# Kernel optimization log

Hardware: AMD Instinct MI355X
Metric: run time of the kernel (lower is better)

Reference implementation:

```python
import jax, jax.numpy as jnp
import numpy as np

N = 100000       # nodes
D_IN = 256       # input feature dim
HID = 128        # hidden dim (GCN output)
D_OUT = 64       # SGCL output dim
NNZ = 1600000    # nnz of gcn adjacency
E = 500000       # directed edges (adj_e)
BIE = 1000000    # bidirectional edges (adj_n)


def setup_inputs() -> dict:
    key = jax.random.key(0)
    ks = jax.random.split(key, 13)
    X = jax.random.normal(ks[0], (N, D_IN), jnp.float32)
    # weight scales chosen so exp(logstd) stays well-conditioned (glorot-like)
    W_gcn = jax.random.normal(ks[1], (D_IN, HID), jnp.float32) * 0.05
    W_miu = jax.random.normal(ks[2], (2 * HID, D_OUT), jnp.float32) * 0.01
    W_sigma = jax.random.normal(ks[3], (2 * HID, D_OUT), jnp.float32) * 0.01
    gcn_values = jax.random.uniform(ks[4], (NNZ,), jnp.float32)
    bi_values = jax.random.uniform(ks[5], (BIE,), jnp.float32)
    noise_in = jax.random.normal(ks[6], (E, D_OUT), jnp.float32)
    noise_out = jax.random.normal(ks[7], (E, D_OUT), jnp.float32)
    noise_node = jax.random.normal(ks[8], (N, D_OUT), jnp.float32)
    gcn_indices = jax.random.randint(ks[9], (2, NNZ), 0, N)
    di_edges = jax.random.randint(ks[10], (2, E), 0, N)
    # ensure every node has at least one incident bi-edge (source side) so that
    # log(aggregated variance) is finite, as with a real symmetric adjacency
    bi_src = jnp.concatenate([jnp.arange(N), jax.random.randint(ks[11], (BIE - N,), 0, N)])
    bi_dst = jax.random.randint(ks[12], (BIE,), 0, N)
    bi_edges = jnp.stack([bi_src, bi_dst], axis=0)
    return {
        "X": X, "W_gcn": W_gcn, "W_miu": W_miu, "W_sigma": W_sigma,
        "gcn_values": gcn_values, "bi_values": bi_values,
        "noise_in": noise_in, "noise_out": noise_out, "noise_node": noise_node,
        "gcn_indices": gcn_indices, "di_edges": di_edges, "bi_edges": bi_edges,
    }


def reference(X, W_gcn, W_miu, W_sigma, gcn_values, bi_values,
              noise_in, noise_out, noise_node, gcn_indices, di_edges, bi_edges):
    n = X.shape[0]
    hid = W_gcn.shape[1]
    # ---- GraphConvSparse with identity activation: adj @ (X @ W) ----
    xw = X @ W_gcn                                     # [N, HID]
    msgs = gcn_values[:, None] * xw[gcn_indices[1]]    # [NNZ, HID]
    hidden = jax.ops.segment_sum(msgs, gcn_indices[0], num_segments=n)
    # split weights: concat([h_a, h_b]) @ W == h_a @ W_top + h_b @ W_bot
    Wm_t, Wm_b = W_miu[:hid], W_miu[hid:]
    Ws_t, Ws_b = W_sigma[:hid], W_sigma[hid:]
    # ---- edge embedding (directed edges) ----
    h_src = hidden[di_edges[0]]                        # [E, HID]
    h_dst = hidden[di_edges[1]]                        # [E, HID]
    miu_in = h_src @ Wm_t + h_dst @ Wm_b               # [E, D_OUT]
    miu_out = h_dst @ Wm_t + h_src @ Wm_b
    logstd_in = h_src @ Ws_t + h_dst @ Ws_b
    logstd_out = h_dst @ Ws_t + h_src @ Ws_b
    edge_in = noise_in * jnp.exp(logstd_in) + miu_in
    edge_out = noise_out * jnp.exp(logstd_out) + miu_out
    # ---- node embedding (bidirectional edges, weighted scatter-aggregate) ----
    b0 = hidden[bi_edges[0]]                           # [BIE, HID]
    b1 = hidden[bi_edges[1]]
    bi_miu = b0 @ Wm_t + b1 @ Wm_b                     # [BIE, D_OUT]
    bi_logstd = b0 @ Ws_t + b1 @ Ws_b
    node_miu = jax.ops.segment_sum(bi_values[:, None] * bi_miu, bi_edges[0], num_segments=n)
    node_var = jax.ops.segment_sum((bi_values ** 2)[:, None] * jnp.exp(bi_logstd), bi_edges[0], num_segments=n)
    node_logstd = 0.5 * jnp.log(node_var)
    node_embed = noise_node * jnp.exp(node_logstd) + node_miu
    return (node_embed, edge_in, edge_out)
```

## Files before the change

kernel.cpp:

```cpp
#include <hip/hip_runtime.h>
#include <hip/hip_bf16.h>
#include <string.h>

typedef unsigned short u16t;
typedef unsigned int   u32t;
typedef unsigned long long u64t;

#define NNODE 100000
#define DIN   256
#define HIDN  128
#define DOUTN 64
#define NNZE  1600000
#define EDIR  500000
#define EBI   1000000
#define G64   1563
#define NBIN  782
#define CH3   4096
#define K3G   391
#define K3B   245
#define KPART (K3G+K3B)
#define CAPG  2432
#define CAPB  1536
#define EBLK  15625

typedef __attribute__((ext_vector_type(8))) short bf16x8;
typedef __attribute__((ext_vector_type(4))) float f32x4;
typedef __attribute__((ext_vector_type(4))) float f4v;

__device__ __forceinline__ u32t pk2bf(float a, float b){
  __hip_bfloat162 h = __float22bfloat162_rn(make_float2(a, b));
  union { __hip_bfloat162 h2; u32t u; } c; c.h2 = h; return c.u;
}
__device__ __forceinline__ u16t s2bf(float a){
  __hip_bfloat16 h = __float2bfloat16(a);
  union { __hip_bfloat16 h1; u16t u; } c; c.h1 = h; return c.u;
}
__device__ __forceinline__ float2 up2(u32t w){
  return make_float2(__uint_as_float(w<<16), __uint_as_float(w&0xFFFF0000u));
}

__global__ __launch_bounds__(256) void histprep_kernel(const int* __restrict__ gi,
                                                       const int* __restrict__ be,
                                                       u32t* __restrict__ gcnt_c,
                                                       u32t* __restrict__ bcnt_c,
                                                       const float* __restrict__ Wg,
                                                       const float* __restrict__ Wm,
                                                       const float* __restrict__ Wsg,
                                                       u16t* __restrict__ Wg_pre,
                                                       u16t* __restrict__ Wc_pre){
  __shared__ u32t h[1024];
  int blk = blockIdx.x, t = threadIdx.x;
  if(blk >= KPART){
    int idx = (blk-KPART)*256 + t;
    int e = idx & 7, l = (idx>>3) & 63, f = (idx>>9) & 63, sel = idx>>15;
    int k_in = ((e>>2)<<4) + ((l>>4)<<2) + (e&3);
    if(sel == 0){
      int ks = f>>3, nf = f&7;
      int k = ks*32 + k_in, n = nf*16 + (l&15);
      Wg_pre[idx] = s2bf(Wg[(size_t)k*HIDN + n]);
    } else {
      int ks = f>>4, nf = f&15;
      int k = ks*32 + k_in, c = nf*16 + (l&15);
      int half = c>>7, ci = c&127;
      const float* src = (ci&1) ? Wsg : Wm;
      Wc_pre[idx - 32768] = s2bf(src[(size_t)(half*128 + k)*DOUTN + (ci>>1)]);
    }
    return;
  }
  const int* keys; u32t* outc; int E, e0;
  if(blk < K3G){ keys=gi; outc=gcnt_c; E=NNZE; e0=blk*CH3; }
  else         { keys=be; outc=bcnt_c; E=EBI;  e0=(blk-K3G)*CH3; }
  for(int i=t;i<1024;i+=256) h[i]=0;
  __syncthreads();
  for(int i=t;i<CH3;i+=256){
    int e=e0+i;
    if(e<E) atomicAdd(&h[(u32t)keys[e]>>7], 1u);
  }
  __syncthreads();
  for(int b=t;b<1024;b+=256){
    u32t c=h[b];
    if(c) atomicAdd(&outc[b], c);
  }
}

__global__ __launch_bounds__(256) void scan_coarse_kernel(u32t* __restrict__ gcnt_c,
                                                          u32t* __restrict__ gcoff,
                                                          u32t* __restrict__ gcur_,
                                                          u32t* __restrict__ bcnt_c,
                                                          u32t* __restrict__ bcoff,
                                                          u32t* __restrict__ bcur_){
  __shared__ u32t part[256];
  u32t *cnt, *coff, *cur;
  if(blockIdx.x==0){ cnt=gcnt_c; coff=gcoff; cur=gcur_; }
  else             { cnt=bcnt_c; coff=bcoff; cur=bcur_; }
  int t = threadIdx.x;
  u32t ch[4], s=0;
  #pragma unroll
  for(int j=0;j<4;j++){ int idx=t*4+j; ch[j] = (idx<NBIN)? cnt[idx] : 0u; s+=ch[j]; }
  part[t]=s; __syncthreads();
  for(int off=1;off<256;off<<=1){
    u32t x=(t>=off)?part[t-off]:0u;
    __syncthreads();
    part[t]+=x;
    __syncthreads();
  }
  u32t run=(t==0)?0u:part[t-1];
  #pragma unroll
  for(int j=0;j<4;j++){
    int idx=t*4+j;
    if(idx<NBIN){ coff[idx]=run; cur[idx]=run; run+=ch[j]; }
  }
  if(t==255) coff[NBIN]=part[255];
}

__global__ __launch_bounds__(256) void partgemm1_kernel(const float* __restrict__ X,
                                                        const u16t* __restrict__ Wg_pre,
                                                        u16t* __restrict__ xwb,
                                                        const int* __restrict__ gi,
                                                        const float* __restrict__ gv,
                                                        const int* __restrict__ be,
                                                        const float* __restrict__ bv,
                                                        u32t* __restrict__ gcur_,
                                                        u64t* __restrict__ gbuck,
                                                        u32t* __restrict__ bcur_,
                                                        u64t* __restrict__ bbuck){
  __shared__ __align__(16) char smem[50176];
  const int t = threadIdx.x;
  if(blockIdx.x < G64){
    u16t* Xs = (u16t*)smem;
    const int l = t & 63, w = t >> 6;
    const int row0 = blockIdx.x * 64;
    for(int i=0;i<16;i++){
      int m = w*16 + i;
      int mg = min(row0 + m, NNODE-1);
      f4v f = __builtin_nontemporal_load((const f4v*)&X[(size_t)mg*DIN + l*4]);
      u32t* p = (u32t*)&Xs[m*256 + ((l ^ (m&15))<<2)];
      p[0] = pk2bf(f[0], f[1]);
      p[1] = pk2bf(f[2], f[3]);
    }
    __syncthreads();
    f32x4 acc[8];
    #pragma unroll
    for(int nf=0;nf<8;nf++) acc[nf] = (f32x4)(0.f);
    const int lm = l & 15, l4 = l >> 4;
    const int mrow = w*16 + lm;
    #pragma unroll 1
    for(int ks=0; ks<8; ks++){
      int kg = ks*8 + l4;
      union { uint2 u2[2]; bf16x8 v; } a;
      a.u2[0] = *(const uint2*)&Xs[mrow*256 + ((kg     ^ lm)<<2)];
      a.u2[1] = *(const uint2*)&Xs[mrow*256 + (((kg+4) ^ lm)<<2)];
      #pragma unroll
      for(int nf=0;nf<8;nf++){
        union { uint4 u4; bf16x8 v; } b;
        b.u4 = *(const uint4*)&Wg_pre[(size_t)((ks*8+nf)*64 + l)*8];
        acc[nf] = __builtin_amdgcn_mfma_f32_16x16x32_bf16(a.v, b.v, acc[nf], 0, 0, 0);
      }
    }
    #pragma unroll
    for(int r=0;r<4;r++){
      int gr = row0 + w*16 + l4*4 + r;
      if(gr < NNODE){
        #pragma unroll
        for(int nf=0;nf<8;nf++)
          xwb[(size_t)gr*HIDN + nf*16 + lm] = s2bf(acc[nf][r]);
      }
    }
    return;
  }
  u32t* hist = (u32t*)smem;
  u32t* scn  = (u32t*)(smem+4096);
  u32t* prt  = (u32t*)(smem+8192);
  u64t* ebuf = (u64t*)(smem+9216);
  u16t* bins = (u16t*)(smem+41984);
  int blk = blockIdx.x - G64;
  const int *keys, *pay; const float* val; u32t* cursor; u64t* buck; int E, e0;
  if(blk < K3G){ keys=gi; pay=gi+NNZE; val=gv; cursor=gcur_; buck=gbuck; E=NNZE; e0=blk*CH3; }
  else         { keys=be; pay=be+EBI;  val=bv; cursor=bcur_; buck=bbuck; E=EBI;  e0=(blk-K3G)*CH3; }
  for(int i=t;i<1024;i+=256) hist[i]=0;
  __syncthreads();
  for(int i=t;i<CH3;i+=256){
    int e=e0+i;
    if(e<E) atomicAdd(&hist[(u32t)keys[e]>>7], 1u);
  }
  __syncthreads();
  u32t ch[4], s=0;
  #pragma unroll
  for(int j=0;j<4;j++){ ch[j]=hist[t*4+j]; s+=ch[j]; }
  prt[t]=s; __syncthreads();
  for(int off=1;off<256;off<<=1){
    u32t x=(t>=off)?prt[t-off]:0u;
    __syncthreads();
    prt[t]+=x;
    __syncthreads();
  }
  u32t run=(t==0)?0u:prt[t-1];
  #pragma unroll
  for(int j=0;j<4;j++){ scn[t*4+j]=run; run+=ch[j]; }
  __syncthreads();
  for(int i=t;i<1024;i+=256) hist[i]=scn[i];
  __syncthreads();
  for(int i=t;i<CH3;i+=256){
    int e=e0+i;
    if(e<E){
      int k = keys[e];
      u32t b = (u32t)k>>7;
      u32t p = atomicAdd(&hist[b],1u);
      u64t ent = (u64t)((u32t)pay[e] | (((u32t)k&127u)<<20)) | ((u64t)__float_as_uint(val[e])<<32);
      ebuf[p]=ent; bins[p]=(u16t)b;
    }
  }
  __syncthreads();
  for(int b=t;b<1024;b+=256){
    u32t c = hist[b]-scn[b];
    u32t bs = c ? atomicAdd(&cursor[b], c) : 0u;
    hist[b] = bs;
  }
  __syncthreads();
  int totalValid = prt[255];
  for(int i=t;i<totalValid;i+=256){
    u32t b = bins[i];
    buck[ (size_t)hist[b] + (u32t)i - scn[b] ] = ebuf[i];
  }
}

__global__ __launch_bounds__(256) void gcn_gather2_kernel(const u16t* __restrict__ xwb,
                                                          const u64t* __restrict__ gbuck,
                                                          const u32t* __restrict__ gcoff,
                                                          u32t* __restrict__ hiddenw){
  __shared__ u64t ebuf[CAPG];
  __shared__ u32t hist[128], offs[129], cur[128], sc[128];
  int bin = blockIdx.x, t = threadIdx.x;
  u32t base = gcoff[bin], cnt = gcoff[bin+1] - base;
  if(t<128) hist[t]=0;
  __syncthreads();
  for(u32t i=t;i<cnt;i+=256)
    atomicAdd(&hist[(u32t)(gbuck[base+i]>>20)&127u], 1u);
  __syncthreads();
  if(t<128) sc[t]=hist[t];
  __syncthreads();
  for(int off=1;off<128;off<<=1){
    u32t x=(t>=off&&t<128)?sc[t-off]:0u;
    __syncthreads();
    if(t<128) sc[t]+=x;
    __syncthreads();
  }
  if(t<128){ offs[t+1]=sc[t]; cur[t]=sc[t]-hist[t]; if(t==0) offs[0]=0u; }
  __syncthreads();
  for(u32t i=t;i<cnt;i+=256){
    u64t e = gbuck[base+i];
    u32t p = atomicAdd(&cur[(u32t)(e>>20)&127u], 1u);
    ebuf[p]=e;
  }
  __syncthreads();
  int w=t>>6, l=t&63;
  const u32t* xww=(const u32t*)xwb;
  for(int idx=w; idx<128; idx+=4){
    int n = bin*128 + idx;
    if(n >= NNODE) continue;
    u32t s0=offs[idx], cnt2=offs[idx+1]-s0;
    float acc0=0.f, acc1=0.f;
    u32t nbr=(cnt2+7)&~7u;
    for(u32t j=0;j<nbr;j+=8){
      float2 xs[8]; float vs[8];
      #pragma unroll
      for(int q=0;q<8;q++){
        u32t jj=j+q;
        u64t e=(jj<cnt2)? ebuf[s0+jj] : 0ULL;
        vs[q]=__uint_as_float((u32t)(e>>32));
        xs[q]=up2(xww[(size_t)(e&0x1FFFFu)*64 + l]);
      }
      #pragma unroll
      for(int q=0;q<8;q++){ acc0+=vs[q]*xs[q].x; acc1+=vs[q]*xs[q].y; }
    }
    hiddenw[(size_t)n*64 + l] = pk2bf(acc0, acc1);
  }
}

__global__ __launch_bounds__(256) void gemm2_kernel(u32t* __restrict__ hiddenw,
                                                    const u16t* __restrict__ Wc_pre,
                                                    u16t* __restrict__ DSTw){
  __shared__ __align__(16) u16t Hs[64*128];
  const int t = threadIdx.x, l = t & 63, w = t >> 6;
  const int row0 = blockIdx.x * 64;
  for(int i=0;i<16;i++){
    int m = w*16 + i;
    int mg = min(row0 + m, NNODE-1);
    u32t v = hiddenw[(size_t)mg*64 + l];
    *(u32t*)&Hs[m*128 + (((l>>1) ^ (m&15))<<2) + ((l&1)<<1)] = v;
  }
  __syncthreads();
  f32x4 acc[16];
  #pragma unroll
  for(int nf=0;nf<16;nf++) acc[nf] = (f32x4)(0.f);
  const int lm = l & 15, l4 = l >> 4;
  const int mrow = w*16 + lm;
  #pragma unroll 1
  for(int ks=0; ks<4; ks++){
    int kg = ks*8 + l4;
    union { uint2 u2[2]; bf16x8 v; } a;
    a.u2[0] = *(const uint2*)&Hs[mrow*128 + ((kg     ^ lm)<<2)];
    a.u2[1] = *(const uint2*)&Hs[mrow*128 + (((kg+4) ^ lm)<<2)];
    #pragma unroll
    for(int nf=0;nf<16;nf++){
      union { uint4 u4; bf16x8 v; } b;
      b.u4 = *(const uint4*)&Wc_pre[(size_t)((ks*16+nf)*64 + l)*8];
      acc[nf] = __builtin_amdgcn_mfma_f32_16x16x32_bf16(a.v, b.v, acc[nf], 0, 0, 0);
    }
  }
  u16t* SRCw = (u16t*)hiddenw;
  #pragma unroll
  for(int r=0;r<4;r++){
    int gr = row0 + w*16 + l4*4 + r;
    if(gr < NNODE){
      #pragma unroll
      for(int nf=0;nf<8;nf++)
        SRCw[(size_t)gr*HIDN + nf*16 + lm] = s2bf(acc[nf][r]);
      #pragma unroll
      for(int nf=8;nf<16;nf++)
        DSTw[(size_t)gr*HIDN + (nf-8)*16 + lm] = s2bf(acc[nf][r]);
    }
  }
}

__global__ __launch_bounds__(256) void edgebi2_kernel(const u16t* __restrict__ SRCb,
                                                      const u16t* __restrict__ DSTb,
                                                      const int*  __restrict__ ed,
                                                      const float* __restrict__ nin,
                                                      const float* __restrict__ nout,
                                                      float* __restrict__ ein,
                                                      float* __restrict__ eout,
                                                      const u64t* __restrict__ bbuck,
                                                      const u32t* __restrict__ bcoff,
                                                      const float* __restrict__ nn,
                                                      float* __restrict__ outp){
  __shared__ u64t ebuf[CAPB];
  __shared__ u32t hist[128], offs[129], cur[128], sc[128];
  const int t = threadIdx.x;
  const u32t* Sw = (const u32t*)SRCb;
  const u32t* Dw = (const u32t*)DSTb;
  if(blockIdx.x >= NBIN){
    const int e0 = ((int)(blockIdx.x - NBIN)*4 + (t>>6))*8;
    const int l = t & 63;
    int s[8], d[8];
    #pragma unroll
    for(int q=0;q<8;q++){ s[q] = ed[e0+q]; d[q] = ed[EDIR+e0+q]; }
    float2 Ss[8], Ds[8], Sd[8], Dd[8];
    float ni[8], no[8];
    #pragma unroll
    for(int q=0;q<8;q++){
      Ss[q] = up2(Sw[(size_t)s[q]*64 + l]);
      Ds[q] = up2(Dw[(size_t)s[q]*64 + l]);
      Sd[q] = up2(Sw[(size_t)d[q]*64 + l]);
      Dd[q] = up2(Dw[(size_t)d[q]*64 + l]);
      ni[q] = __builtin_nontemporal_load(&nin[(size_t)(e0+q)*DOUTN + l]);
      no[q] = __builtin_nontemporal_load(&nout[(size_t)(e0+q)*DOUTN + l]);
    }
    #pragma unroll
    for(int q=0;q<8;q++){
      size_t o = (size_t)(e0+q)*DOUTN + l;
      float miu_in  = Ss[q].x + Dd[q].x, ls_in  = Ss[q].y + Dd[q].y;
      float miu_out = Sd[q].x + Ds[q].x, ls_out = Sd[q].y + Ds[q].y;
      __builtin_nontemporal_store(ni[q] * __expf(ls_in)  + miu_in,  &ein[o]);
      __builtin_nontemporal_store(no[q] * __expf(ls_out) + miu_out, &eout[o]);
    }
    return;
  }
  int bin = blockIdx.x;
  u32t base = bcoff[bin], cnt = bcoff[bin+1] - base;
  if(t<128) hist[t]=0;
  __syncthreads();
  for(u32t i=t;i<cnt;i+=256)
    atomicAdd(&hist[(u32t)(bbuck[base+i]>>20)&127u], 1u);
  __syncthreads();
  if(t<128) sc[t]=hist[t];
  __syncthreads();
  for(int off=1;off<128;off<<=1){
    u32t x=(t>=off&&t<128)?sc[t-off]:0u;
    __syncthreads();
    if(t<128) sc[t]+=x;
    __syncthreads();
  }
  if(t<128){ offs[t+1]=sc[t]; cur[t]=sc[t]-hist[t]; if(t==0) offs[0]=0u; }
  __syncthreads();
  for(u32t i=t;i<cnt;i+=256){
    u64t e = bbuck[base+i];
    u32t p = atomicAdd(&cur[(u32t)(e>>20)&127u], 1u);
    ebuf[p]=e;
  }
  __syncthreads();
  int w=t>>6, l=t&63;
  for(int idx=w; idx<128; idx+=4){
    int n = bin*128 + idx;
    if(n >= NNODE) continue;
    float2 S = up2(Sw[(size_t)n*64 + l]);
    u32t s0=offs[idx], cnt2=offs[idx+1]-s0;
    float nmiu=0.f, nvar=0.f;
    u32t nbr=(cnt2+3)&~3u;
    for(u32t j=0;j<nbr;j+=4){
      float2 Dq[4]; float vs[4];
      #pragma unroll
      for(int q=0;q<4;q++){
        u32t jj=j+q;
        u64t e=(jj<cnt2)? ebuf[s0+jj] : 0ULL;
        vs[q]=__uint_as_float((u32t)(e>>32));
        Dq[q]=up2(Dw[(size_t)(e&0x1FFFFu)*64 + l]);
      }
      #pragma unroll
      for(int q=0;q<4;q++){
        nmiu += vs[q]*(S.x+Dq[q].x);
        nvar += vs[q]*vs[q]*__expf(S.y+Dq[q].y);
      }
    }
    size_t o = (size_t)n*DOUTN + l;
    float nd = __builtin_nontemporal_load(&nn[o]);
    __builtin_nontemporal_store(nd*sqrtf(nvar) + nmiu, &outp[o]);
  }
}

extern "C" void kernel_launch(void* const* d_in, const int* in_sizes, int n_in,
                              void* d_out, int out_size, void* d_ws, size_t ws_size,
                              hipStream_t stream){
  const float* X    = (const float*)d_in[0];
  const float* Wg   = (const float*)d_in[1];
  const float* Wm   = (const float*)d_in[2];
  const float* Wsg  = (const float*)d_in[3];
  const float* gv   = (const float*)d_in[4];
  const float* bv   = (const float*)d_in[5];
  const float* nin  = (const float*)d_in[6];
  const float* nout = (const float*)d_in[7];
  const float* nnod = (const float*)d_in[8];
  const int*  gi   = (const int*)d_in[9];
  const int*  ed   = (const int*)d_in[10];
  const int*  be   = (const int*)d_in[11];

  char* ws = (char*)d_ws;
  u64t*  gbuck   = (u64t*)ws;
  u16t*  xwb     = (u16t*)(ws + 12800000);
  u32t*  gcnt_c  = (u32t*)(ws + 38400000);
  u32t*  bcnt_c  = (u32t*)(ws + 38404096);
  u32t*  gcoff   = (u32t*)(ws + 38408192);
  u32t*  gcur_   = (u32t*)(ws + 38412288);
  u32t*  bcoff   = (u32t*)(ws + 38416384);
  u32t*  bcur_   = (u32t*)(ws + 38420480);
  u64t*  bbuck   = (u64t*)(ws + 40003168);
  u32t*  hiddenw = (u32t*)(ws + 51200000);
  u16t*  SRCw    = (u16t*)hiddenw;
  u16t*  DSTw    = (u16t*)ws;

  float* out  = (float*)d_out;
  float* ein  = out + (size_t)NNODE*DOUTN;
  float* eout = ein + (size_t)EDIR*DOUTN;
  u16t* Wg_pre = (u16t*)((char*)d_out + 25600000 - 131072);
  u16t* Wc_pre = Wg_pre + 32768;

  (void)hipMemsetAsync(gcnt_c, 0, 8192, stream);
  histprep_kernel   <<<KPART+256, 256, 0, stream>>>(gi, be, gcnt_c, bcnt_c,
                                                    Wg, Wm, Wsg, Wg_pre, Wc_pre);
  scan_coarse_kernel<<<2,         256, 0, stream>>>(gcnt_c, gcoff, gcur_, bcnt_c, bcoff, bcur_);
  partgemm1_kernel  <<<G64+KPART, 256, 0, stream>>>(X, Wg_pre, xwb,
                                                    gi, gv, be, bv, gcur_, gbuck, bcur_, bbuck);
  gcn_gather2_kernel<<<NBIN,      256, 0, stream>>>(xwb, gbuck, gcoff, hiddenw);
  gemm2_kernel      <<<G64,       256, 0, stream>>>(hiddenw, Wc_pre, DSTw);
  edgebi2_kernel    <<<NBIN+EBLK, 256, 0, stream>>>(SRCw, DSTw, ed, nin, nout,
                                                    ein, eout, bbuck, bcoff, nnod, out);
}
```

Measured before the change: 383.8 us.

## Bucket directed edges by source node and stage source rows in LDS

Directed edges are now bucket-sorted by source node bin, reusing the existing histogram, scan and partition pipeline. Each edge block loads its 128 source rows of the SRC and DST projections into shared memory once, so only the destination gathers go to global memory. The change is meant to cut random gather traffic on the edge path. In exchange it adds partition work, a large shared-memory footprint per block (which lowers occupancy for the node blocks too), and noise reads and output writes that are now scattered by edge id instead of streamed.

```diff
diff --git a/kernel.cpp b/kernel.cpp
--- a/kernel.cpp
+++ b/kernel.cpp
@@ -1,6 +1,5 @@
 #include <hip/hip_runtime.h>
 #include <hip/hip_bf16.h>
-#include <string.h>
 
 typedef unsigned short u16t;
 typedef unsigned int   u32t;
@@ -18,10 +17,11 @@
 #define CH3   4096
 #define K3G   391
 #define K3B   245
-#define KPART (K3G+K3B)
+#define K3E   123
+#define KPART (K3G+K3B+K3E)
 #define CAPG  2432
 #define CAPB  1536
-#define EBLK  15625
+#define CAPE  896
 
 typedef __attribute__((ext_vector_type(8))) short bf16x8;
 typedef __attribute__((ext_vector_type(4))) float f32x4;
@@ -41,8 +41,10 @@
 
 __global__ __launch_bounds__(256) void histprep_kernel(const int* __restrict__ gi,
                                                        const int* __restrict__ be,
+                                                       const int* __restrict__ ed,
                                                        u32t* __restrict__ gcnt_c,
                                                        u32t* __restrict__ bcnt_c,
+                                                       u32t* __restrict__ ecnt_c,
                                                        const float* __restrict__ Wg,
                                                        const float* __restrict__ Wm,
                                                        const float* __restrict__ Wsg,
@@ -68,8 +70,9 @@
     return;
   }
   const int* keys; u32t* outc; int E, e0;
-  if(blk < K3G){ keys=gi; outc=gcnt_c; E=NNZE; e0=blk*CH3; }
-  else         { keys=be; outc=bcnt_c; E=EBI;  e0=(blk-K3G)*CH3; }
+  if(blk < K3G)          { keys=gi; outc=gcnt_c; E=NNZE; e0=blk*CH3; }
+  else if(blk < K3G+K3B) { keys=be; outc=bcnt_c; E=EBI;  e0=(blk-K3G)*CH3; }
+  else                   { keys=ed; outc=ecnt_c; E=EDIR; e0=(blk-K3G-K3B)*CH3; }
   for(int i=t;i<1024;i+=256) h[i]=0;
   __syncthreads();
   for(int i=t;i<CH3;i+=256){
@@ -88,11 +91,15 @@
                                                           u32t* __restrict__ gcur_,
                                                           u32t* __restrict__ bcnt_c,
                                                           u32t* __restrict__ bcoff,
-                                                          u32t* __restrict__ bcur_){
+                                                          u32t* __restrict__ bcur_,
+                                                          u32t* __restrict__ ecnt_c,
+                                                          u32t* __restrict__ ecoff,
+                                                          u32t* __restrict__ ecur_){
   __shared__ u32t part[256];
   u32t *cnt, *coff, *cur;
-  if(blockIdx.x==0){ cnt=gcnt_c; coff=gcoff; cur=gcur_; }
-  else             { cnt=bcnt_c; coff=bcoff; cur=bcur_; }
+  if(blockIdx.x==0)      { cnt=gcnt_c; coff=gcoff; cur=gcur_; }
+  else if(blockIdx.x==1) { cnt=bcnt_c; coff=bcoff; cur=bcur_; }
+  else                   { cnt=ecnt_c; coff=ecoff; cur=ecur_; }
   int t = threadIdx.x;
   u32t ch[4], s=0;
   #pragma unroll
@@ -120,10 +127,13 @@
                                                         const float* __restrict__ gv,
                                                         const int* __restrict__ be,
                                                         const float* __restrict__ bv,
+                                                        const int* __restrict__ ed,
                                                         u32t* __restrict__ gcur_,
                                                         u64t* __restrict__ gbuck,
                                                         u32t* __restrict__ bcur_,
-                                                        u64t* __restrict__ bbuck){
+                                                        u64t* __restrict__ bbuck,
+                                                        u32t* __restrict__ ecur_,
+                                                        u64t* __restrict__ ebuck){
   __shared__ __align__(16) char smem[50176];
   const int t = threadIdx.x;
   if(blockIdx.x < G64){
@@ -174,9 +184,10 @@
   u64t* ebuf = (u64t*)(smem+9216);
   u16t* bins = (u16t*)(smem+41984);
   int blk = blockIdx.x - G64;
-  const int *keys, *pay; const float* val; u32t* cursor; u64t* buck; int E, e0;
-  if(blk < K3G){ keys=gi; pay=gi+NNZE; val=gv; cursor=gcur_; buck=gbuck; E=NNZE; e0=blk*CH3; }
-  else         { keys=be; pay=be+EBI;  val=bv; cursor=bcur_; buck=bbuck; E=EBI;  e0=(blk-K3G)*CH3; }
+  const int *keys, *pay; const float* val; u32t* cursor; u64t* buck; int E, e0; bool eStream=false;
+  if(blk < K3G)          { keys=gi; pay=gi+NNZE; val=gv; cursor=gcur_; buck=gbuck; E=NNZE; e0=blk*CH3; }
+  else if(blk < K3G+K3B) { keys=be; pay=be+EBI;  val=bv; cursor=bcur_; buck=bbuck; E=EBI;  e0=(blk-K3G)*CH3; }
+  else                   { keys=ed; pay=ed+EDIR; val=0;  cursor=ecur_; buck=ebuck; E=EDIR; e0=(blk-K3G-K3B)*CH3; eStream=true; }
   for(int i=t;i<1024;i+=256) hist[i]=0;
   __syncthreads();
   for(int i=t;i<CH3;i+=256){
@@ -206,7 +217,8 @@
       int k = keys[e];
       u32t b = (u32t)k>>7;
       u32t p = atomicAdd(&hist[b],1u);
-      u64t ent = (u64t)((u32t)pay[e] | (((u32t)k&127u)<<20)) | ((u64t)__float_as_uint(val[e])<<32);
+      u64t hi = eStream ? (u64t)(u32t)e : (u64t)__float_as_uint(val[e]);
+      u64t ent = (u64t)((u32t)pay[e] | (((u32t)k&127u)<<20)) | (hi<<32);
       ebuf[p]=ent; bins[p]=(u16t)b;
     }
   }
@@ -325,47 +337,75 @@
 
 __global__ __launch_bounds__(256) void edgebi2_kernel(const u16t* __restrict__ SRCb,
                                                       const u16t* __restrict__ DSTb,
-                                                      const int*  __restrict__ ed,
                                                       const float* __restrict__ nin,
                                                       const float* __restrict__ nout,
                                                       float* __restrict__ ein,
                                                       float* __restrict__ eout,
                                                       const u64t* __restrict__ bbuck,
                                                       const u32t* __restrict__ bcoff,
+                                                      const u64t* __restrict__ ebuck,
+                                                      const u32t* __restrict__ ecoff,
                                                       const float* __restrict__ nn,
                                                       float* __restrict__ outp){
-  __shared__ u64t ebuf[CAPB];
-  __shared__ u32t hist[128], offs[129], cur[128], sc[128];
+  __shared__ __align__(16) char smem2[72704];
   const int t = threadIdx.x;
   const u32t* Sw = (const u32t*)SRCb;
   const u32t* Dw = (const u32t*)DSTb;
+  const int w = t>>6, l = t&63;
   if(blockIdx.x >= NBIN){
-    const int e0 = ((int)(blockIdx.x - NBIN)*4 + (t>>6))*8;
-    const int l = t & 63;
-    int s[8], d[8];
-    #pragma unroll
-    for(int q=0;q<8;q++){ s[q] = ed[e0+q]; d[q] = ed[EDIR+e0+q]; }
-    float2 Ss[8], Ds[8], Sd[8], Dd[8];
-    float ni[8], no[8];
-    #pragma unroll
-    for(int q=0;q<8;q++){
-      Ss[q] = up2(Sw[(size_t)s[q]*64 + l]);
-      Ds[q] = up2(Dw[(size_t)s[q]*64 + l]);
-      Sd[q] = up2(Sw[(size_t)d[q]*64 + l]);
-      Dd[q] = up2(Dw[(size_t)d[q]*64 + l]);
-      ni[q] = __builtin_nontemporal_load(&nin[(size_t)(e0+q)*DOUTN + l]);
-      no[q] = __builtin_nontemporal_load(&nout[(size_t)(e0+q)*DOUTN + l]);
-    }
-    #pragma unroll
-    for(int q=0;q<8;q++){
-      size_t o = (size_t)(e0+q)*DOUTN + l;
-      float miu_in  = Ss[q].x + Dd[q].x, ls_in  = Ss[q].y + Dd[q].y;
-      float miu_out = Sd[q].x + Ds[q].x, ls_out = Sd[q].y + Ds[q].y;
-      __builtin_nontemporal_store(ni[q] * __expf(ls_in)  + miu_in,  &ein[o]);
-      __builtin_nontemporal_store(no[q] * __expf(ls_out) + miu_out, &eout[o]);
+    u32t* Sst  = (u32t*)smem2;
+    u32t* Dst_ = (u32t*)(smem2+32768);
+    u64t* ent  = (u64t*)(smem2+65536);
+    int bin = blockIdx.x - NBIN;
+    u32t base = ecoff[bin], cnt = ecoff[bin+1] - base;
+    u32t cntp = (cnt+7)&~7u;
+    for(u32t i=t;i<cntp;i+=256) ent[i] = (i<cnt)? ebuck[base+i] : 0ULL;
+    for(int r=w; r<128; r+=4){
+      int n = bin*128 + r;
+      if(n < NNODE){
+        Sst[r*64+l]  = Sw[(size_t)n*64 + l];
+        Dst_[r*64+l] = Dw[(size_t)n*64 + l];
+      }
+    }
+    __syncthreads();
+    for(u32t i0 = (u32t)w*8; i0 < cnt; i0 += 32){
+      u32t eq[8], dq[8], slq[8];
+      #pragma unroll
+      for(int q=0;q<8;q++){
+        u64t en = ent[i0+q];
+        u32t lo = (u32t)en;
+        eq[q]  = (u32t)(en>>32);
+        dq[q]  = lo & 0x1FFFFu;
+        slq[q] = (lo>>20)&127u;
+      }
+      float2 Ssq[8], Dsq[8], Sdq[8], Ddq[8]; float niq[8], noq[8];
+      #pragma unroll
+      for(int q=0;q<8;q++){
+        Ssq[q] = up2(Sst[slq[q]*64 + l]);
+        Dsq[q] = up2(Dst_[slq[q]*64 + l]);
+        Sdq[q] = up2(Sw[(size_t)dq[q]*64 + l]);
+        Ddq[q] = up2(Dw[(size_t)dq[q]*64 + l]);
+        niq[q] = __builtin_nontemporal_load(&nin[(size_t)eq[q]*DOUTN + l]);
+        noq[q] = __builtin_nontemporal_load(&nout[(size_t)eq[q]*DOUTN + l]);
+      }
+      #pragma unroll
+      for(int q=0;q<8;q++){
+        if(i0 + (u32t)q < cnt){
+          size_t o = (size_t)eq[q]*DOUTN + l;
+          float miu_in  = Ssq[q].x + Ddq[q].x, ls_in  = Ssq[q].y + Ddq[q].y;
+          float miu_out = Sdq[q].x + Dsq[q].x, ls_out = Sdq[q].y + Dsq[q].y;
+          __builtin_nontemporal_store(niq[q] * __expf(ls_in)  + miu_in,  &ein[o]);
+          __builtin_nontemporal_store(noq[q] * __expf(ls_out) + miu_out, &eout[o]);
+        }
+      }
     }
     return;
   }
+  u64t* ebuf = (u64t*)smem2;
+  u32t* hist = (u32t*)(smem2+12288);
+  u32t* offs = (u32t*)(smem2+12800);
+  u32t* cur  = (u32t*)(smem2+13328);
+  u32t* sc   = (u32t*)(smem2+13840);
   int bin = blockIdx.x;
   u32t base = bcoff[bin], cnt = bcoff[bin+1] - base;
   if(t<128) hist[t]=0;
@@ -389,7 +429,6 @@
     ebuf[p]=e;
   }
   __syncthreads();
-  int w=t>>6, l=t&63;
   for(int idx=w; idx<128; idx+=4){
     int n = bin*128 + idx;
     if(n >= NNODE) continue;
@@ -439,11 +478,15 @@
   u16t*  xwb     = (u16t*)(ws + 12800000);
   u32t*  gcnt_c  = (u32t*)(ws + 38400000);
   u32t*  bcnt_c  = (u32t*)(ws + 38404096);
-  u32t*  gcoff   = (u32t*)(ws + 38408192);
-  u32t*  gcur_   = (u32t*)(ws + 38412288);
-  u32t*  bcoff   = (u32t*)(ws + 38416384);
-  u32t*  bcur_   = (u32t*)(ws + 38420480);
-  u64t*  bbuck   = (u64t*)(ws + 40003168);
+  u32t*  ecnt_c  = (u32t*)(ws + 38408192);
+  u32t*  gcoff   = (u32t*)(ws + 38412288);
+  u32t*  gcur_   = (u32t*)(ws + 38416384);
+  u32t*  bcoff   = (u32t*)(ws + 38420480);
+  u32t*  bcur_   = (u32t*)(ws + 38424576);
+  u32t*  ecoff   = (u32t*)(ws + 38428672);
+  u32t*  ecur_   = (u32t*)(ws + 38432768);
+  u64t*  bbuck   = (u64t*)(ws + 38440000);
+  u64t*  ebuck   = (u64t*)(ws + 46440000);
   u32t*  hiddenw = (u32t*)(ws + 51200000);
   u16t*  SRCw    = (u16t*)hiddenw;
   u16t*  DSTw    = (u16t*)ws;
@@ -454,14 +497,17 @@
   u16t* Wg_pre = (u16t*)((char*)d_out + 25600000 - 131072);
   u16t* Wc_pre = Wg_pre + 32768;
 
-  (void)hipMemsetAsync(gcnt_c, 0, 8192, stream);
-  histprep_kernel   <<<KPART+256, 256, 0, stream>>>(gi, be, gcnt_c, bcnt_c,
+  (void)hipMemsetAsync(gcnt_c, 0, 12288, stream);
+  histprep_kernel   <<<KPART+256, 256, 0, stream>>>(gi, be, ed, gcnt_c, bcnt_c, ecnt_c,
                                                     Wg, Wm, Wsg, Wg_pre, Wc_pre);
-  scan_coarse_kernel<<<2,         256, 0, stream>>>(gcnt_c, gcoff, gcur_, bcnt_c, bcoff, bcur_);
+  scan_coarse_kernel<<<3,         256, 0, stream>>>(gcnt_c, gcoff, gcur_, bcnt_c, bcoff, bcur_,
+                                                    ecnt_c, ecoff, ecur_);
   partgemm1_kernel  <<<G64+KPART, 256, 0, stream>>>(X, Wg_pre, xwb,
-                                                    gi, gv, be, bv, gcur_, gbuck, bcur_, bbuck);
+                                                    gi, gv, be, bv, ed,
+                                                    gcur_, gbuck, bcur_, bbuck, ecur_, ebuck);
   gcn_gather2_kernel<<<NBIN,      256, 0, stream>>>(xwb, gbuck, gcoff, hiddenw);
   gemm2_kernel      <<<G64,       256, 0, stream>>>(hiddenw, Wc_pre, DSTw);
-  edgebi2_kernel    <<<NBIN+EBLK, 256, 0, stream>>>(SRCw, DSTw, ed, nin, nout,
-                                                    ein, eout, bbuck, bcoff, nnod, out);
-}
+  edgebi2_kernel    <<<2*NBIN,    256, 0, stream>>>(SRCw, DSTw, nin, nout,
+                                                    ein, eout, bbuck, bcoff,
+                                                    ebuck, ecoff, nnod, out);
+}
```

Result: slower. 481.5 us (+25.4%).
